# Kernel optimization log

Hardware: AMD Instinct MI355X
Metric: run time of the kernel (lower is better)

Reference implementation:

```python
import jax, jax.numpy as jnp
import numpy as np

B, L, LO, H, V = 8, 1024, 1024, 768, 4096
NUM_TAGS = 256


def _merge_one(tags):
    """Replicates merge_weights() for one sequence of tags [L].

    A maximal run of equal, non-(-1) tags becomes one output row that averages
    the hidden states over the run. A run is only emitted when it is *closed*
    by a tag change or a -1 (so a run ending at the last position is dropped,
    exactly like the torch loop). Remaining rows are zero with bias -100.
    """
    Ls = tags.shape[0]
    pos = jnp.arange(Ls)
    valid = tags != -1
    prev = jnp.concatenate([jnp.full((1,), -2, tags.dtype), tags[:-1]])
    start = valid & ((pos == 0) | (tags != prev) | (prev == -1))
    seg_id = jnp.cumsum(start.astype(jnp.int32)) - 1          # run index per position
    total_runs = seg_id[-1] + 1
    emitted = total_runs - valid[-1].astype(jnp.int32)        # trailing open run dropped
    seg_clip = jnp.clip(seg_id, 0, Ls - 1)
    # run lengths via segment sum (invalid positions contribute 0)
    counts = jax.ops.segment_sum(valid.astype(jnp.float32), seg_clip, num_segments=Ls)
    w = jnp.where(valid & (seg_id >= 0) & (seg_id < emitted),
                  1.0 / jnp.maximum(counts[seg_clip], 1.0), 0.0)
    merge = jnp.zeros((Ls, Ls), jnp.float32).at[seg_clip, pos].add(w)  # [rows, tokens]
    bias = jnp.where(pos < emitted, 0.0, -100.0)
    return merge, bias


def setup_inputs() -> dict:
    key = jax.random.key(0)
    k1, k2, k3, k4 = jax.random.split(key, 4)
    hidden1_states = jax.random.normal(k1, (B, L, H), jnp.float32)
    hidden2_states = jax.random.normal(k2, (B, LO, H), jnp.float32)
    lm_logits = jax.random.normal(k3, (B, LO, V), jnp.float32)
    tags = jnp.sort(jax.random.randint(k4, (B, L), 0, NUM_TAGS), axis=-1)
    return {"hidden1_states": hidden1_states, "hidden2_states": hidden2_states,
            "lm_logits": lm_logits, "tags": tags}


def reference(hidden1_states, hidden2_states, lm_logits, tags):
    merge, bias = jax.vmap(_merge_one)(tags)                     # [B,L,L], [B,L]
    attn = jnp.einsum('bls,bsh->blh', merge, hidden1_states)     # segment means
    attn1 = jnp.einsum('boh,blh->bol', hidden2_states, attn) + bias[:, None, :]
    return jnp.concatenate([lm_logits, attn1], axis=2)           # [B,LO,V+L]
```

## Files before the change

kernel.cpp:

```cpp
#include <hip/hip_runtime.h>
#include <hip/hip_bf16.h>
#include <stdint.h>

#define BB   8
#define LL   1024
#define LOO  1024
#define HH   768
#define VV   4096
#define OUTW 5120
#define EMAX 256

typedef unsigned short ushort_t;
typedef __attribute__((ext_vector_type(4))) float   f32x4;
typedef __attribute__((ext_vector_type(8))) __bf16  bf16x8;
typedef __attribute__((ext_vector_type(4))) float   float4v;
typedef __attribute__((ext_vector_type(4))) int     int4v;
typedef __attribute__((ext_vector_type(4))) unsigned short ushort4v;

static __device__ __forceinline__ ushort_t f2bf(float f) {
    union { float f; uint32_t u; } v; v.f = f;
    uint32_t u = v.u;
    uint32_t r = (u + 0x7fffu + ((u >> 16) & 1u)) >> 16;
    return (ushort_t)r;
}

__global__ __launch_bounds__(256) void attn_fused_kernel(
        const float* __restrict__ h1,
        const int* __restrict__ tags,
        ushort_t* __restrict__ attn,
        int* __restrict__ emitted_out) {
    int b = blockIdx.x >> 8;
    int r = blockIdx.x & 255;
    int tid = threadIdx.x;

    __shared__ int stags[LL];
    __shared__ int cnt[256];
    __shared__ int runpos[EMAX + 2];

    ((int4v*)stags)[tid] = ((const int4v*)(tags + b * LL))[tid];
    __syncthreads();

    int p0 = tid * 4;
    int st[4];
    int prevm1 = (p0 == 0) ? -2 : stags[p0 - 1];
    st[0] = (p0 == 0) || (stags[p0] != prevm1);
    st[1] = (stags[p0 + 1] != stags[p0]);
    st[2] = (stags[p0 + 2] != stags[p0 + 1]);
    st[3] = (stags[p0 + 3] != stags[p0 + 2]);
    int c = st[0] + st[1] + st[2] + st[3];
    cnt[tid] = c;
    __syncthreads();
    for (int off = 1; off < 256; off <<= 1) {
        int v = cnt[tid];
        int a = (tid >= off) ? cnt[tid - off] : 0;
        __syncthreads();
        cnt[tid] = v + a;
        __syncthreads();
    }
    int total = cnt[255];
    int base = cnt[tid] - c;
#pragma unroll
    for (int j = 0; j < 4; ++j)
        if (st[j]) runpos[base++] = p0 + j;
    if (tid == 0) runpos[total] = LL;
    __syncthreads();

    int em = total - 1;
    if (r == 0 && tid == 0) emitted_out[b] = em;

    ushort_t* arow = attn + ((size_t)b * EMAX + r) * HH;
    if (r >= em) {
        arow[tid] = 0; arow[tid + 256] = 0; arow[tid + 512] = 0;
        return;
    }
    int s = runpos[r], e = runpos[r + 1];
    float inv = 1.0f / (float)(e - s);
    const float* hb = h1 + (size_t)b * LL * HH;
    float a0 = 0.f, a1 = 0.f, a2 = 0.f;
    for (int p = s; p < e; ++p) {
        const float* row = hb + (size_t)p * HH;
        a0 += row[tid]; a1 += row[tid + 256]; a2 += row[tid + 512];
    }
    arow[tid]       = f2bf(a0 * inv);
    arow[tid + 256] = f2bf(a1 * inv);
    arow[tid + 512] = f2bf(a2 * inv);
}

__global__ __launch_bounds__(256, 4) void fused_out_kernel(
        const float* __restrict__ h2,
        const ushort_t* __restrict__ Bm,
        const int* __restrict__ emitted,
        const float* __restrict__ lm,
        float* __restrict__ out) {
    __shared__ char smem[34816];

    const int bid = blockIdx.x;
    const int b   = bid >> 6;
    const int r0  = (bid & 63) << 4;

    const int tid  = threadIdx.x;
    const int lane = tid & 63;
    const int w    = tid >> 6;

    const float*    Ab = h2 + ((size_t)b * LOO + r0) * HH;
    const ushort_t* Bb = Bm + (size_t)b * EMAX * HH;

    f32x4 zero = {0.f, 0.f, 0.f, 0.f};
    f32x4 acc[4];
    acc[0] = zero; acc[1] = zero; acc[2] = zero; acc[3] = zero;

    const int arow_s = tid >> 4;
    const int akq    = tid & 15;
    for (int k0 = 0; k0 < HH; k0 += 64) {
        __syncthreads();
        {
            f32x4 v = *(const f32x4*)(Ab + (size_t)arow_s * HH + k0 + akq * 4);
            ushort4v o;
            o[0] = f2bf(v[0]); o[1] = f2bf(v[1]); o[2] = f2bf(v[2]); o[3] = f2bf(v[3]);
            *(ushort4v*)(smem + arow_s * 128 + ((akq * 8) ^ ((arow_s & 7) << 4))) = o;
        }
#pragma unroll
        for (int i = 0; i < 8; ++i) {
            int off = i * 4096 + tid * 16;
            int row = off >> 7;
            int cb  = off & 127;
            int scb = cb ^ ((row & 7) << 4);
            const ushort_t* gb = Bb + (size_t)row * HH + k0 + (scb >> 1);
            __builtin_amdgcn_global_load_lds(
                (const __attribute__((address_space(1))) void*)gb,
                (__attribute__((address_space(3))) void*)(smem + 2048 + off), 16, 0, 0);
        }
        asm volatile("s_waitcnt vmcnt(0)" ::: "memory");
        __syncthreads();

#pragma unroll
        for (int ks = 0; ks < 2; ++ks) {
            int kb   = (ks << 6) + ((lane >> 4) << 4);
            int ar   = lane & 15;
            bf16x8 af = *(const bf16x8*)(smem + ar * 128 + (kb ^ ((ar & 7) << 4)));
#pragma unroll
            for (int ni = 0; ni < 4; ++ni) {
                int br = ((w << 2) + ni) * 16 + (lane & 15);
                bf16x8 bf = *(const bf16x8*)(smem + 2048 + br * 128 + (kb ^ ((br & 7) << 4)));
                acc[ni] = __builtin_amdgcn_mfma_f32_16x16x32_bf16(af, bf, acc[ni], 0, 0, 0);
            }
        }
    }

    {
        int em = emitted[b];
        float* outb = out + ((size_t)b * LOO + r0) * OUTW + VV;
#pragma unroll
        for (int ni = 0; ni < 4; ++ni) {
            int l = ((w << 2) + ni) * 16 + (lane & 15);
            float badd = (l < em) ? 0.0f : -100.0f;
            int rbase = (lane >> 4) << 2;
#pragma unroll
            for (int rr = 0; rr < 4; ++rr)
                outb[(size_t)(rbase + rr) * OUTW + l] = acc[ni][rr] + badd;
        }
    }

    const float4v* lm4 = (const float4v*)lm + ((size_t)b * LOO + r0) * (VV / 4);
    float4v* o4 = (float4v*)out + ((size_t)b * LOO + r0) * (OUTW / 4);
    float4v fv = {-100.f, -100.f, -100.f, -100.f};
#pragma unroll 2
    for (int r = 0; r < 16; ++r) {
        float4v v0 = __builtin_nontemporal_load(&lm4[r * 1024 + tid]);
        float4v v1 = __builtin_nontemporal_load(&lm4[r * 1024 + tid + 256]);
        float4v v2 = __builtin_nontemporal_load(&lm4[r * 1024 + tid + 512]);
        float4v v3 = __builtin_nontemporal_load(&lm4[r * 1024 + tid + 768]);
        __builtin_nontemporal_store(v0, &o4[r * 1280 + tid]);
        __builtin_nontemporal_store(v1, &o4[r * 1280 + tid + 256]);
        __builtin_nontemporal_store(v2, &o4[r * 1280 + tid + 512]);
        __builtin_nontemporal_store(v3, &o4[r * 1280 + tid + 768]);
        if (tid < 192)
            __builtin_nontemporal_store(fv, &o4[r * 1280 + 1088 + tid]);
    }
}

extern "C" void kernel_launch(void* const* d_in, const int* in_sizes, int n_in,
                              void* d_out, int out_size, void* d_ws, size_t ws_size,
                              hipStream_t stream) {
    const float* h1   = (const float*)d_in[0];
    const float* h2   = (const float*)d_in[1];
    const float* lm   = (const float*)d_in[2];
    const int*   tags = (const int*)d_in[3];
    float* out = (float*)d_out;

    char* ws = (char*)d_ws;
    ushort_t* attn    = (ushort_t*)ws;
    int*      emitted = (int*)(ws + 3145728);

    attn_fused_kernel<<<BB * EMAX, 256, 0, stream>>>(h1, tags, attn, emitted);
    fused_out_kernel<<<512, 256, 0, stream>>>(h2, attn, emitted, lm, out);
}
```

Baseline: 86.32 us.

## Fuse segment-mean and GEMM kernels into one persistent kernel with per-batch spin barrier

Merges the run-averaging kernel and the output GEMM/copy kernel into a single launch of 512 blocks. Each block recomputes the run boundaries with wave shuffles, computes two averaged rows per wave, then signals a per-batch atomic counter and spins until all 128 contributors finish before running the GEMM. Two waves per block stream the lm_logits copy concurrently while the other two do the MFMA work with 16x128 tiles per wave. This removes a kernel launch and overlaps the copy with compute. It relies on all 64 blocks of a batch being co-resident to avoid deadlock, and it adds a memset launch.

```diff
diff --git a/kernel.cpp b/kernel.cpp
--- a/kernel.cpp
+++ b/kernel.cpp
@@ -15,7 +15,6 @@
 typedef __attribute__((ext_vector_type(8))) __bf16  bf16x8;
 typedef __attribute__((ext_vector_type(4))) float   float4v;
 typedef __attribute__((ext_vector_type(4))) int     int4v;
-typedef __attribute__((ext_vector_type(4))) unsigned short ushort4v;
 
 static __device__ __forceinline__ ushort_t f2bf(float f) {
     union { float f; uint32_t u; } v; v.f = f;
@@ -24,158 +23,189 @@
     return (ushort_t)r;
 }
 
-__global__ __launch_bounds__(256) void attn_fused_kernel(
+__global__ __launch_bounds__(256) void fused_all_kernel(
         const float* __restrict__ h1,
-        const int* __restrict__ tags,
-        ushort_t* __restrict__ attn,
-        int* __restrict__ emitted_out) {
-    int b = blockIdx.x >> 8;
-    int r = blockIdx.x & 255;
-    int tid = threadIdx.x;
-
-    __shared__ int stags[LL];
-    __shared__ int cnt[256];
-    __shared__ int runpos[EMAX + 2];
-
-    ((int4v*)stags)[tid] = ((const int4v*)(tags + b * LL))[tid];
-    __syncthreads();
-
-    int p0 = tid * 4;
-    int st[4];
-    int prevm1 = (p0 == 0) ? -2 : stags[p0 - 1];
-    st[0] = (p0 == 0) || (stags[p0] != prevm1);
-    st[1] = (stags[p0 + 1] != stags[p0]);
-    st[2] = (stags[p0 + 2] != stags[p0 + 1]);
-    st[3] = (stags[p0 + 3] != stags[p0 + 2]);
-    int c = st[0] + st[1] + st[2] + st[3];
-    cnt[tid] = c;
-    __syncthreads();
-    for (int off = 1; off < 256; off <<= 1) {
-        int v = cnt[tid];
-        int a = (tid >= off) ? cnt[tid - off] : 0;
-        __syncthreads();
-        cnt[tid] = v + a;
-        __syncthreads();
-    }
-    int total = cnt[255];
-    int base = cnt[tid] - c;
-#pragma unroll
-    for (int j = 0; j < 4; ++j)
-        if (st[j]) runpos[base++] = p0 + j;
-    if (tid == 0) runpos[total] = LL;
-    __syncthreads();
-
-    int em = total - 1;
-    if (r == 0 && tid == 0) emitted_out[b] = em;
-
-    ushort_t* arow = attn + ((size_t)b * EMAX + r) * HH;
-    if (r >= em) {
-        arow[tid] = 0; arow[tid + 256] = 0; arow[tid + 512] = 0;
-        return;
-    }
-    int s = runpos[r], e = runpos[r + 1];
-    float inv = 1.0f / (float)(e - s);
-    const float* hb = h1 + (size_t)b * LL * HH;
-    float a0 = 0.f, a1 = 0.f, a2 = 0.f;
-    for (int p = s; p < e; ++p) {
-        const float* row = hb + (size_t)p * HH;
-        a0 += row[tid]; a1 += row[tid + 256]; a2 += row[tid + 512];
-    }
-    arow[tid]       = f2bf(a0 * inv);
-    arow[tid + 256] = f2bf(a1 * inv);
-    arow[tid + 512] = f2bf(a2 * inv);
-}
-
-__global__ __launch_bounds__(256, 4) void fused_out_kernel(
         const float* __restrict__ h2,
-        const ushort_t* __restrict__ Bm,
-        const int* __restrict__ emitted,
         const float* __restrict__ lm,
-        float* __restrict__ out) {
-    __shared__ char smem[34816];
-
-    const int bid = blockIdx.x;
-    const int b   = bid >> 6;
-    const int r0  = (bid & 63) << 4;
-
+        const int*   __restrict__ tags,
+        ushort_t*    __restrict__ attn,
+        int*         __restrict__ done,
+        float*       __restrict__ out) {
+    __shared__ char smem[36864];
+
+    const int bid  = blockIdx.x;
+    const int b    = bid >> 6;
+    const int rg   = bid & 63;
+    const int r0   = rg << 4;
     const int tid  = threadIdx.x;
     const int lane = tid & 63;
     const int w    = tid >> 6;
 
+    const float4v* lm4 = (const float4v*)lm + ((size_t)b * LOO + r0) * (VV / 4);
+    float4v*       o4  = (float4v*)out + ((size_t)b * LOO + r0) * (OUTW / 4);
+    const float4v  fv  = {-100.f, -100.f, -100.f, -100.f};
+
+    if (w >= 2) {
+        for (int r = (w - 2) * 6; r < (w - 2) * 6 + 6; ++r) {
+#pragma unroll
+            for (int it = 0; it < 16; it += 4) {
+                float4v v0 = __builtin_nontemporal_load(&lm4[r * 1024 + (it + 0) * 64 + lane]);
+                float4v v1 = __builtin_nontemporal_load(&lm4[r * 1024 + (it + 1) * 64 + lane]);
+                float4v v2 = __builtin_nontemporal_load(&lm4[r * 1024 + (it + 2) * 64 + lane]);
+                float4v v3 = __builtin_nontemporal_load(&lm4[r * 1024 + (it + 3) * 64 + lane]);
+                __builtin_nontemporal_store(v0, &o4[r * 1280 + (it + 0) * 64 + lane]);
+                __builtin_nontemporal_store(v1, &o4[r * 1280 + (it + 1) * 64 + lane]);
+                __builtin_nontemporal_store(v2, &o4[r * 1280 + (it + 2) * 64 + lane]);
+                __builtin_nontemporal_store(v3, &o4[r * 1280 + (it + 3) * 64 + lane]);
+            }
+#pragma unroll
+            for (int it = 0; it < 3; ++it)
+                __builtin_nontemporal_store(fv, &o4[r * 1280 + 1088 + it * 64 + lane]);
+        }
+        return;
+    }
+
+    char* Aw = smem + w * 18432;
+    char* Bw = smem + w * 18432 + 2048;
+
+    const int* tg = tags + b * LL;
+    int p0 = lane * 16;
+    int tvv[17];
+    tvv[0] = (lane == 0) ? -2 : tg[p0 - 1];
+#pragma unroll
+    for (int q = 0; q < 4; ++q) {
+        int4v t4 = ((const int4v*)(tg + p0))[q];
+        tvv[1 + 4 * q] = t4[0]; tvv[2 + 4 * q] = t4[1];
+        tvv[3 + 4 * q] = t4[2]; tvv[4 + 4 * q] = t4[3];
+    }
+    int st_[16], c = 0;
+#pragma unroll
+    for (int i = 0; i < 16; ++i) { st_[i] = (tvv[i + 1] != tvv[i]); c += st_[i]; }
+    int incl = c;
+#pragma unroll
+    for (int off = 1; off < 64; off <<= 1) {
+        int n = __shfl_up(incl, off, 64);
+        if (lane >= off) incl += n;
+    }
+    int total = __shfl(incl, 63, 64);
+    int em    = total - 1;
+    int* runpos = (int*)Aw;
+    int base = incl - c;
+#pragma unroll
+    for (int i = 0; i < 16; ++i)
+        if (st_[i]) runpos[base++] = p0 + i;
+    if (lane == 63) runpos[total] = LL;
+    asm volatile("s_waitcnt lgkmcnt(0)" ::: "memory");
+
+#pragma unroll
+    for (int rr = 0; rr < 2; ++rr) {
+        int r = (rg << 2) + (w << 1) + rr;
+        ushort_t* arow = attn + ((size_t)b * EMAX + r) * HH;
+        if (r >= em) {
+#pragma unroll
+            for (int j = 0; j < 12; ++j) arow[lane + 64 * j] = 0;
+        } else {
+            int s = runpos[r], e = runpos[r + 1];
+            float inv = 1.0f / (float)(e - s);
+            float a[12];
+#pragma unroll
+            for (int j = 0; j < 12; ++j) a[j] = 0.f;
+            for (int p = s; p < e; ++p) {
+                const float* row = h1 + ((size_t)b * LL + p) * HH;
+#pragma unroll
+                for (int j = 0; j < 12; ++j) a[j] += row[lane + 64 * j];
+            }
+#pragma unroll
+            for (int j = 0; j < 12; ++j) arow[lane + 64 * j] = f2bf(a[j] * inv);
+        }
+    }
+
+    if (lane == 0)
+        __hip_atomic_fetch_add(&done[b], 1, __ATOMIC_RELEASE, __HIP_MEMORY_SCOPE_AGENT);
+    while (__hip_atomic_load(&done[b], __ATOMIC_ACQUIRE, __HIP_MEMORY_SCOPE_AGENT) < 128)
+        __builtin_amdgcn_s_sleep(2);
+
     const float*    Ab = h2 + ((size_t)b * LOO + r0) * HH;
-    const ushort_t* Bb = Bm + (size_t)b * EMAX * HH;
-
-    f32x4 zero = {0.f, 0.f, 0.f, 0.f};
-    f32x4 acc[4];
-    acc[0] = zero; acc[1] = zero; acc[2] = zero; acc[3] = zero;
-
-    const int arow_s = tid >> 4;
-    const int akq    = tid & 15;
+    const ushort_t* Bb = attn + (size_t)b * EMAX * HH;
+
+    f32x4 acc[8];
+#pragma unroll
+    for (int i = 0; i < 8; ++i) acc[i] = (f32x4){0.f, 0.f, 0.f, 0.f};
+
     for (int k0 = 0; k0 < HH; k0 += 64) {
-        __syncthreads();
-        {
-            f32x4 v = *(const f32x4*)(Ab + (size_t)arow_s * HH + k0 + akq * 4);
-            ushort4v o;
-            o[0] = f2bf(v[0]); o[1] = f2bf(v[1]); o[2] = f2bf(v[2]); o[3] = f2bf(v[3]);
-            *(ushort4v*)(smem + arow_s * 128 + ((akq * 8) ^ ((arow_s & 7) << 4))) = o;
-        }
-#pragma unroll
-        for (int i = 0; i < 8; ++i) {
-            int off = i * 4096 + tid * 16;
+#pragma unroll
+        for (int i = 0; i < 16; ++i) {
+            int off = i * 1024 + lane * 16;
             int row = off >> 7;
             int cb  = off & 127;
             int scb = cb ^ ((row & 7) << 4);
-            const ushort_t* gb = Bb + (size_t)row * HH + k0 + (scb >> 1);
+            const ushort_t* gb = Bb + (size_t)((w << 7) + row) * HH + k0 + (scb >> 1);
             __builtin_amdgcn_global_load_lds(
                 (const __attribute__((address_space(1))) void*)gb,
-                (__attribute__((address_space(3))) void*)(smem + 2048 + off), 16, 0, 0);
+                (__attribute__((address_space(3))) void*)(Bw + off), 16, 0, 0);
+        }
+        {
+            const float* pa = Ab + (size_t)(lane & 15) * HH + k0 + ((lane >> 4) << 4);
+            f32x4 v0 = ((const f32x4*)pa)[0];
+            f32x4 v1 = ((const f32x4*)pa)[1];
+            f32x4 v2 = ((const f32x4*)pa)[2];
+            f32x4 v3 = ((const f32x4*)pa)[3];
+            bf16x8 t0, t1;
+            t0[0] = (__bf16)v0[0]; t0[1] = (__bf16)v0[1]; t0[2] = (__bf16)v0[2]; t0[3] = (__bf16)v0[3];
+            t0[4] = (__bf16)v1[0]; t0[5] = (__bf16)v1[1]; t0[6] = (__bf16)v1[2]; t0[7] = (__bf16)v1[3];
+            t1[0] = (__bf16)v2[0]; t1[1] = (__bf16)v2[1]; t1[2] = (__bf16)v2[2]; t1[3] = (__bf16)v2[3];
+            t1[4] = (__bf16)v3[0]; t1[5] = (__bf16)v3[1]; t1[6] = (__bf16)v3[2]; t1[7] = (__bf16)v3[3];
+            int ar = lane & 15;
+            int bo = (lane >> 4) << 5;
+            int sw = (ar & 7) << 4;
+            *(bf16x8*)(Aw + ar * 128 + (bo ^ sw))        = t0;
+            *(bf16x8*)(Aw + ar * 128 + ((bo + 16) ^ sw)) = t1;
         }
         asm volatile("s_waitcnt vmcnt(0)" ::: "memory");
-        __syncthreads();
+        __builtin_amdgcn_sched_barrier(0);
 
 #pragma unroll
         for (int ks = 0; ks < 2; ++ks) {
-            int kb   = (ks << 6) + ((lane >> 4) << 4);
-            int ar   = lane & 15;
-            bf16x8 af = *(const bf16x8*)(smem + ar * 128 + (kb ^ ((ar & 7) << 4)));
-#pragma unroll
-            for (int ni = 0; ni < 4; ++ni) {
-                int br = ((w << 2) + ni) * 16 + (lane & 15);
-                bf16x8 bf = *(const bf16x8*)(smem + 2048 + br * 128 + (kb ^ ((br & 7) << 4)));
+            int kb = (ks << 6) + ((lane >> 4) << 4);
+            int ar = lane & 15;
+            bf16x8 af = *(const bf16x8*)(Aw + ar * 128 + (kb ^ ((ar & 7) << 4)));
+#pragma unroll
+            for (int ni = 0; ni < 8; ++ni) {
+                int br = (ni << 4) + (lane & 15);
+                bf16x8 bf = *(const bf16x8*)(Bw + br * 128 + (kb ^ ((br & 7) << 4)));
                 acc[ni] = __builtin_amdgcn_mfma_f32_16x16x32_bf16(af, bf, acc[ni], 0, 0, 0);
             }
         }
     }
 
     {
-        int em = emitted[b];
         float* outb = out + ((size_t)b * LOO + r0) * OUTW + VV;
 #pragma unroll
-        for (int ni = 0; ni < 4; ++ni) {
-            int l = ((w << 2) + ni) * 16 + (lane & 15);
-            float badd = (l < em) ? 0.0f : -100.0f;
+        for (int ni = 0; ni < 8; ++ni) {
+            int col = (w << 7) + (ni << 4) + (lane & 15);
+            float badd = (col < em) ? 0.0f : -100.0f;
             int rbase = (lane >> 4) << 2;
 #pragma unroll
-            for (int rr = 0; rr < 4; ++rr)
-                outb[(size_t)(rbase + rr) * OUTW + l] = acc[ni][rr] + badd;
-        }
-    }
-
-    const float4v* lm4 = (const float4v*)lm + ((size_t)b * LOO + r0) * (VV / 4);
-    float4v* o4 = (float4v*)out + ((size_t)b * LOO + r0) * (OUTW / 4);
-    float4v fv = {-100.f, -100.f, -100.f, -100.f};
-#pragma unroll 2
-    for (int r = 0; r < 16; ++r) {
-        float4v v0 = __builtin_nontemporal_load(&lm4[r * 1024 + tid]);
-        float4v v1 = __builtin_nontemporal_load(&lm4[r * 1024 + tid + 256]);
-        float4v v2 = __builtin_nontemporal_load(&lm4[r * 1024 + tid + 512]);
-        float4v v3 = __builtin_nontemporal_load(&lm4[r * 1024 + tid + 768]);
-        __builtin_nontemporal_store(v0, &o4[r * 1280 + tid]);
-        __builtin_nontemporal_store(v1, &o4[r * 1280 + tid + 256]);
-        __builtin_nontemporal_store(v2, &o4[r * 1280 + tid + 512]);
-        __builtin_nontemporal_store(v3, &o4[r * 1280 + tid + 768]);
-        if (tid < 192)
-            __builtin_nontemporal_store(fv, &o4[r * 1280 + 1088 + tid]);
+            for (int rrr = 0; rrr < 4; ++rrr)
+                outb[(size_t)(rbase + rrr) * OUTW + col] = acc[ni][rrr] + badd;
+        }
+    }
+
+    for (int r = 12 + w * 2; r < 14 + w * 2; ++r) {
+#pragma unroll
+        for (int it = 0; it < 16; it += 4) {
+            float4v v0 = __builtin_nontemporal_load(&lm4[r * 1024 + (it + 0) * 64 + lane]);
+            float4v v1 = __builtin_nontemporal_load(&lm4[r * 1024 + (it + 1) * 64 + lane]);
+            float4v v2 = __builtin_nontemporal_load(&lm4[r * 1024 + (it + 2) * 64 + lane]);
+            float4v v3 = __builtin_nontemporal_load(&lm4[r * 1024 + (it + 3) * 64 + lane]);
+            __builtin_nontemporal_store(v0, &o4[r * 1280 + (it + 0) * 64 + lane]);
+            __builtin_nontemporal_store(v1, &o4[r * 1280 + (it + 1) * 64 + lane]);
+            __builtin_nontemporal_store(v2, &o4[r * 1280 + (it + 2) * 64 + lane]);
+            __builtin_nontemporal_store(v3, &o4[r * 1280 + (it + 3) * 64 + lane]);
+        }
+#pragma unroll
+        for (int it = 0; it < 3; ++it)
+            __builtin_nontemporal_store(fv, &o4[r * 1280 + 1088 + it * 64 + lane]);
     }
 }
 
@@ -189,9 +219,9 @@
     float* out = (float*)d_out;
 
     char* ws = (char*)d_ws;
-    ushort_t* attn    = (ushort_t*)ws;
-    int*      emitted = (int*)(ws + 3145728);
-
-    attn_fused_kernel<<<BB * EMAX, 256, 0, stream>>>(h1, tags, attn, emitted);
-    fused_out_kernel<<<512, 256, 0, stream>>>(h2, attn, emitted, lm, out);
+    ushort_t* attn = (ushort_t*)ws;
+    int*      done = (int*)(ws + 3145728);
+
+    hipMemsetAsync(done, 0, BB * sizeof(int), stream);
+    fused_all_kernel<<<512, 256, 0, stream>>>(h1, h2, lm, tags, attn, done, out);
 }
```

After: 234.3 us. 171% more time.
